# Kernel optimization log

Hardware: AMD Instinct MI355X
Metric: run time of the kernel (lower is better)

## Reference

```python
import jax, jax.numpy as jnp
import numpy as np

B, IN, K, E = 2048, 1024, 128, 64  # batch, in_features, n_concepts, emb_size


def setup_inputs() -> dict:
    key = jax.random.key(0)
    k1, k2, k3, k4, k5 = jax.random.split(key, 5)
    x = jax.random.normal(k1, (B, IN), dtype=jnp.float32)
    # stacked per-concept Linear(in_features, 2*emb_size)
    W = jax.random.normal(k2, (K, IN, 2 * E), dtype=jnp.float32) * (1.0 / np.sqrt(IN))
    b = jax.random.normal(k3, (K, 2 * E), dtype=jnp.float32) * 0.01
    # shared prob predictor Linear(2*emb_size, 1)
    wp = jax.random.normal(k4, (2 * E,), dtype=jnp.float32) * (1.0 / np.sqrt(2 * E))
    bp = jax.random.normal(k5, (), dtype=jnp.float32) * 0.01
    return {"x": x, "W": W, "b": b, "wp": wp, "bp": bp}


def reference(x, W, b, wp, bp):
    # batched GEMM over all concepts at once: [B,K,2E]
    context = jax.nn.leaky_relu(jnp.einsum('bi,kio->bko', x, W) + b)
    # shared predictor + sigmoid: [B,K]
    c_pred = jax.nn.sigmoid(jnp.einsum('bko,o->bk', context, wp) + bp)
    ctx_pos = context[..., :E]
    ctx_neg = context[..., E:]
    p = c_pred[..., None]
    c_emb = ctx_pos * p + ctx_neg * (1.0 - p)  # [B,K,E]
    return c_emb, c_pred
```

## Files before the change

kernel.cpp:

```cpp
#include <hip/hip_runtime.h>

typedef unsigned int u32;
typedef unsigned short u16;
typedef __attribute__((ext_vector_type(8))) __bf16 bf16x8;
typedef __attribute__((ext_vector_type(4))) float f32x4;

#define B_SZ 2048
#define IN_SZ 1024
#define K_SZ 128
#define E_SZ 64
#define TWOE 128
static const size_t OUT_EMB = (size_t)B_SZ * K_SZ * E_SZ;

__device__ __forceinline__ u16 f2bf(float f) {
    u32 u = __builtin_bit_cast(u32, f);
    u32 r = u + 0x7fffu + ((u >> 16) & 1u);
    return (u16)(r >> 16);
}

__device__ __forceinline__ void async16(const void* g, void* l) {
    __builtin_amdgcn_global_load_lds((const __attribute__((address_space(1))) u32*)g,
                                     (__attribute__((address_space(3))) u32*)l, 16, 0, 0);
}

__global__ void __launch_bounds__(256) cvt_x(const float* __restrict__ in, u16* __restrict__ outp, int n4) {
    int i = blockIdx.x * blockDim.x + threadIdx.x;
    if (i < n4) {
        float4 v = ((const float4*)in)[i];
        u32 lo = (u32)f2bf(v.x) | ((u32)f2bf(v.y) << 16);
        u32 hi = (u32)f2bf(v.z) | ((u32)f2bf(v.w) << 16);
        ((uint2*)outp)[i] = make_uint2(lo, hi);
    }
}

__global__ void __launch_bounds__(256) cvt_w(const float* __restrict__ W, u16* __restrict__ wt) {
    __shared__ u16 tr[128][72];
    const int k = blockIdx.y, i0 = blockIdx.x * 64;
    const float* src = W + (size_t)k * IN_SZ * TWOE + (size_t)i0 * TWOE;
#pragma unroll
    for (int r = 0; r < 8; ++r) {
        int idx = r * 256 + threadIdx.x;
        int i = idx >> 5;
        int o = (idx & 31) * 4;
        float4 v = ((const float4*)src)[idx];
        tr[o + 0][i] = f2bf(v.x);
        tr[o + 1][i] = f2bf(v.y);
        tr[o + 2][i] = f2bf(v.z);
        tr[o + 3][i] = f2bf(v.w);
    }
    __syncthreads();
    const int o = threadIdx.x >> 1, h = threadIdx.x & 1;
    u16* dst = wt + ((size_t)(k * TWOE + o) * IN_SZ) + i0 + h * 32;
#pragma unroll
    for (int s = 0; s < 4; ++s) {
        uint4 v = *(const uint4*)&tr[o][h * 32 + s * 8];
        ((uint4*)dst)[s] = v;
    }
}

__global__ void __launch_bounds__(256) cvt_pred(const float* __restrict__ pw, float* __restrict__ out) {
    __shared__ float t[128][132];
    const int b0 = blockIdx.x * 128;
    const int tid = threadIdx.x;
#pragma unroll
    for (int i = 0; i < 16; ++i) {
        int idx = i * 256 + tid;
        int kk = idx >> 5, c4 = (idx & 31) * 4;
        float4 v = *(const float4*)(pw + (size_t)kk * B_SZ + b0 + c4);
        t[kk][c4 + 0] = v.x; t[kk][c4 + 1] = v.y; t[kk][c4 + 2] = v.z; t[kk][c4 + 3] = v.w;
    }
    __syncthreads();
#pragma unroll
    for (int i = 0; i < 16; ++i) {
        int idx = i * 256 + tid;
        int bl = idx >> 5, k4 = (idx & 31) * 4;
        float4 v = make_float4(t[k4 + 0][bl], t[k4 + 1][bl], t[k4 + 2][bl], t[k4 + 3][bl]);
        *(float4*)(out + OUT_EMB + (size_t)(b0 + bl) * K_SZ + k4) = v;
    }
}

__global__ void __launch_bounds__(512, 2) fused_main(
    const u16* __restrict__ xb,
    const u16* __restrict__ wt,
    const float* __restrict__ bias, const float* __restrict__ wpv,
    const float* __restrict__ bpp, float* __restrict__ out,
    float* __restrict__ pw) {
    __shared__ u16 smst[32768];
    char* smb = (char*)&smst[0];

    const int tid = threadIdx.x;
    const int l = tid & 63, w = tid >> 6;
    const int wm = w >> 2, wn = w & 3;
    const int hi = l >> 4, lo16 = l & 15;
    const int q = l >> 2;
    const int swz = (l & 3) ^ ((l >> 3) & 3);

    const int id = blockIdx.x;
    const int xcd = id & 7, j = id >> 3;
    const int kp = (xcd << 3) | (j >> 3);
    const int brow = (j & 7) << 8;

    const u16* abase = wt + ((size_t)kp * 256 + w * 16 + q) * IN_SZ + swz * 8;
    const u16* bbase = xb + (size_t)(brow + w * 16 + q) * IN_SZ + swz * 8;

    const int xsl = (hi ^ ((lo16 >> 1) & 3)) << 4;

    f32x4 acc[8][4] = {};

    auto SA = [&](int d, int tp) {
        u16* dst = &smst[0] + d * 8192 + w * 512;
        const u16* src = abase + tp * 32;
        async16(src, dst);
        async16(src + (size_t)128 * IN_SZ, dst + 4096);
    };
    auto SB = [&](int d, int tp) {
        u16* dst = &smst[0] + 16384 + d * 8192 + w * 512;
        const u16* src = bbase + tp * 32;
        async16(src, dst);
        async16(src + (size_t)128 * IN_SZ, dst + 4096);
    };

    auto PHN = [&](int d) {
        const char* ra = smb + d * 16384;
        const char* rb = smb + 32768 + d * 16384;
        bf16x8 af[8], bfr[4];
#pragma unroll
        for (int n = 0; n < 4; ++n)
            bfr[n] = *(const bf16x8*)(rb + (wn * 64 + n * 16 + lo16) * 64 + xsl);
#pragma unroll
        for (int mm = 0; mm < 8; ++mm)
            af[mm] = *(const bf16x8*)(ra + (wm * 128 + mm * 16 + lo16) * 64 + xsl);
        __builtin_amdgcn_s_setprio(1);
#pragma unroll
        for (int mm = 0; mm < 8; ++mm)
#pragma unroll
            for (int n = 0; n < 4; ++n)
                acc[mm][n] = __builtin_amdgcn_mfma_f32_16x16x32_bf16(
                    af[mm], bfr[n], acc[mm][n], 0, 0, 0);
        __builtin_amdgcn_s_setprio(0);
    };

    SA(0, 0); SB(0, 0);
    asm volatile("s_waitcnt vmcnt(0)" ::: "memory");
    __builtin_amdgcn_s_barrier();

#pragma unroll 1
    for (int t = 0; t < 32; ++t) {
        const int d = t & 1;
        if (t < 31) {
            SA(d ^ 1, t + 1); SB(d ^ 1, t + 1);
            asm volatile("" ::: "memory");
        }
        PHN(d);
        asm volatile("s_waitcnt vmcnt(0)" ::: "memory");
        __builtin_amdgcn_s_barrier();
    }

    const int kglob = kp * 2 + wm;
    const float bp_val = *bpp;
    float4 b4[8], w4[8];
#pragma unroll
    for (int m = 0; m < 8; ++m) {
        b4[m] = *(const float4*)(bias + kglob * TWOE + m * 16 + hi * 4);
        w4[m] = *(const float4*)(wpv + m * 16 + hi * 4);
    }
    float pn[4];
#pragma unroll
    for (int n = 0; n < 4; ++n) {
        float s = 0.f;
#pragma unroll
        for (int m = 0; m < 8; ++m) {
            f32x4 v = acc[m][n];
            float t0 = v[0] + b4[m].x; t0 = t0 > 0.f ? t0 : 0.01f * t0;
            float t1 = v[1] + b4[m].y; t1 = t1 > 0.f ? t1 : 0.01f * t1;
            float t2 = v[2] + b4[m].z; t2 = t2 > 0.f ? t2 : 0.01f * t2;
            float t3 = v[3] + b4[m].w; t3 = t3 > 0.f ? t3 : 0.01f * t3;
            v[0] = t0; v[1] = t1; v[2] = t2; v[3] = t3;
            acc[m][n] = v;
            s += t0 * w4[m].x + t1 * w4[m].y + t2 * w4[m].z + t3 * w4[m].w;
        }
        s += __shfl_xor(s, 16);
        s += __shfl_xor(s, 32);
        pn[n] = 1.f / (1.f + __expf(-(s + bp_val)));
    }
    if (hi == 0) {
        if (pw) {
#pragma unroll
            for (int n = 0; n < 4; ++n)
                pw[(size_t)kglob * B_SZ + brow + wn * 64 + n * 16 + lo16] = pn[n];
        } else {
#pragma unroll
            for (int n = 0; n < 4; ++n)
                out[OUT_EMB + (size_t)(brow + wn * 64 + n * 16 + lo16) * K_SZ + kglob] = pn[n];
        }
    }
#pragma unroll
    for (int n = 0; n < 4; ++n) {
        const size_t bb = (size_t)(brow + wn * 64 + n * 16 + lo16);
        float* op = out + (bb * K_SZ + kglob) * E_SZ + hi * 4;
        const float pv = pn[n], qv = 1.f - pn[n];
#pragma unroll
        for (int mp = 0; mp < 4; ++mp) {
            f32x4 cp = acc[mp][n], cn = acc[mp + 4][n];
            f32x4 r;
            r[0] = pv * cp[0] + qv * cn[0];
            r[1] = pv * cp[1] + qv * cn[1];
            r[2] = pv * cp[2] + qv * cn[2];
            r[3] = pv * cp[3] + qv * cn[3];
            *(f32x4*)(op + mp * 16) = r;
        }
    }
}

__global__ void __launch_bounds__(128) fallback_kernel(
    const float* __restrict__ x, const float* __restrict__ W,
    const float* __restrict__ bias, const float* __restrict__ wpv,
    const float* __restrict__ bpp, float* __restrict__ out) {
    const int k = blockIdx.y;
    const int b0 = blockIdx.x * 8;
    const int o = threadIdx.x;
    __shared__ float xs[8][1024];
    __shared__ float red[2];
    __shared__ float exch[64];
    for (int idx = threadIdx.x; idx < 8 * 1024; idx += 128)
        xs[idx >> 10][idx & 1023] = x[(size_t)(b0 + (idx >> 10)) * IN_SZ + (idx & 1023)];
    __syncthreads();
    float a[8] = {};
    for (int i = 0; i < 1024; ++i) {
        float wv = W[((size_t)k * IN_SZ + i) * TWOE + o];
#pragma unroll
        for (int bb = 0; bb < 8; ++bb) a[bb] += xs[bb][i] * wv;
    }
    const float bo = bias[k * TWOE + o], wo = wpv[o], bpv = *bpp;
    for (int bb = 0; bb < 8; ++bb) {
        float c = a[bb] + bo;
        c = c > 0.f ? c : 0.01f * c;
        float s = c * wo;
        for (int off = 1; off < 64; off <<= 1) s += __shfl_xor(s, off);
        if ((threadIdx.x & 63) == 0) red[threadIdx.x >> 6] = s;
        __syncthreads();
        float p = 1.f / (1.f + expf(-(red[0] + red[1] + bpv)));
        if (o >= 64) exch[o - 64] = (1.f - p) * c;
        __syncthreads();
        if (o < 64) out[((size_t)(b0 + bb) * K_SZ + k) * E_SZ + o] = p * c + exch[o];
        if (o == 0) out[OUT_EMB + (size_t)(b0 + bb) * K_SZ + k] = p;
        __syncthreads();
    }
}

extern "C" void kernel_launch(void* const* d_in, const int* in_sizes, int n_in,
                              void* d_out, int out_size, void* d_ws, size_t ws_size,
                              hipStream_t stream) {
    const float* x = (const float*)d_in[0];
    const float* W = (const float*)d_in[1];
    const float* bias = (const float*)d_in[2];
    const float* wp = (const float*)d_in[3];
    const float* bp = (const float*)d_in[4];
    float* out = (float*)d_out;

    const size_t X_ELEMS = (size_t)B_SZ * IN_SZ;
    const size_t WT_ELEMS = (size_t)K_SZ * TWOE * IN_SZ;
    const size_t PW_ELEMS = (size_t)K_SZ * B_SZ;
    const size_t NEED_BASE = (X_ELEMS + WT_ELEMS) * sizeof(u16);
    const size_t NEED_FULL = NEED_BASE + PW_ELEMS * sizeof(float);

    if (ws_size >= NEED_BASE) {
        u16* xb = (u16*)d_ws;
        u16* wt = xb + X_ELEMS;
        float* pw = (ws_size >= NEED_FULL) ? (float*)(wt + WT_ELEMS) : nullptr;
        int n4 = (int)(X_ELEMS / 4);
        cvt_x<<<dim3((n4 + 255) / 256), 256, 0, stream>>>(x, xb, n4);
        cvt_w<<<dim3(16, 128), 256, 0, stream>>>(W, wt);
        fused_main<<<dim3(512), 512, 0, stream>>>(xb, wt, bias, wp, bp, out, pw);
        if (pw) cvt_pred<<<dim3(16), 256, 0, stream>>>(pw, out);
    } else {
        fallback_kernel<<<dim3(B_SZ / 8, K_SZ), 128, 0, stream>>>(x, W, bias, wp, bp, out);
    }
}
```

Baseline: 108.4 us.

## Merge x/W bf16 conversion kernels and deepen GEMM prefetch to two stages

Combines the separate x and W fp32→bf16 conversion kernels into one launch with extra grid rows for x, removing one kernel launch and its tail. The main GEMM loop now prefetches two K-tiles ahead. Each iteration issues the load for tile t+2 into the buffer it has just read into registers, then waits with vmcnt(4) instead of vmcnt(0), so global loads overlap more with the MFMA work. The cost is an extra barrier per iteration after the LDS reads, plus the need for correct vmcnt accounting.

```diff
diff --git a/kernel.cpp b/kernel.cpp
--- a/kernel.cpp
+++ b/kernel.cpp
@@ -23,38 +23,43 @@
                                      (__attribute__((address_space(3))) u32*)l, 16, 0, 0);
 }
 
-__global__ void __launch_bounds__(256) cvt_x(const float* __restrict__ in, u16* __restrict__ outp, int n4) {
-    int i = blockIdx.x * blockDim.x + threadIdx.x;
-    if (i < n4) {
-        float4 v = ((const float4*)in)[i];
-        u32 lo = (u32)f2bf(v.x) | ((u32)f2bf(v.y) << 16);
-        u32 hi = (u32)f2bf(v.z) | ((u32)f2bf(v.w) << 16);
-        ((uint2*)outp)[i] = make_uint2(lo, hi);
-    }
-}
-
-__global__ void __launch_bounds__(256) cvt_w(const float* __restrict__ W, u16* __restrict__ wt) {
-    __shared__ u16 tr[128][72];
-    const int k = blockIdx.y, i0 = blockIdx.x * 64;
-    const float* src = W + (size_t)k * IN_SZ * TWOE + (size_t)i0 * TWOE;
-#pragma unroll
-    for (int r = 0; r < 8; ++r) {
-        int idx = r * 256 + threadIdx.x;
-        int i = idx >> 5;
-        int o = (idx & 31) * 4;
-        float4 v = ((const float4*)src)[idx];
-        tr[o + 0][i] = f2bf(v.x);
-        tr[o + 1][i] = f2bf(v.y);
-        tr[o + 2][i] = f2bf(v.z);
-        tr[o + 3][i] = f2bf(v.w);
-    }
-    __syncthreads();
-    const int o = threadIdx.x >> 1, h = threadIdx.x & 1;
-    u16* dst = wt + ((size_t)(k * TWOE + o) * IN_SZ) + i0 + h * 32;
-#pragma unroll
-    for (int s = 0; s < 4; ++s) {
-        uint4 v = *(const uint4*)&tr[o][h * 32 + s * 8];
-        ((uint4*)dst)[s] = v;
+__global__ void __launch_bounds__(256) cvt_xw(const float* __restrict__ W, u16* __restrict__ wt,
+                                              const float* __restrict__ x, u16* __restrict__ xb) {
+    const int tid = threadIdx.x;
+    if (blockIdx.y < 128) {
+        __shared__ u16 tr[128][72];
+        const int k = blockIdx.y, i0 = blockIdx.x * 64;
+        const float* src = W + (size_t)k * IN_SZ * TWOE + (size_t)i0 * TWOE;
+#pragma unroll
+        for (int r = 0; r < 8; ++r) {
+            int idx = r * 256 + tid;
+            int i = idx >> 5;
+            int o = (idx & 31) * 4;
+            float4 v = ((const float4*)src)[idx];
+            tr[o + 0][i] = f2bf(v.x);
+            tr[o + 1][i] = f2bf(v.y);
+            tr[o + 2][i] = f2bf(v.z);
+            tr[o + 3][i] = f2bf(v.w);
+        }
+        __syncthreads();
+        const int o = tid >> 1, h = tid & 1;
+        u16* dst = wt + ((size_t)(k * TWOE + o) * IN_SZ) + i0 + h * 32;
+#pragma unroll
+        for (int s = 0; s < 4; ++s) {
+            uint4 v = *(const uint4*)&tr[o][h * 32 + s * 8];
+            ((uint4*)dst)[s] = v;
+        }
+    } else {
+        const int chunk = (blockIdx.y - 128) * 16 + blockIdx.x;
+        const int base = chunk * 4096;
+#pragma unroll
+        for (int s = 0; s < 16; ++s) {
+            int i = base + s * 256 + tid;
+            float4 v = ((const float4*)x)[i];
+            u32 lo = (u32)f2bf(v.x) | ((u32)f2bf(v.y) << 16);
+            u32 hi = (u32)f2bf(v.z) | ((u32)f2bf(v.w) << 16);
+            ((uint2*)xb)[i] = make_uint2(lo, hi);
+        }
     }
 }
 
@@ -120,7 +125,14 @@
         async16(src + (size_t)128 * IN_SZ, dst + 4096);
     };
 
-    auto PHN = [&](int d) {
+    SA(0, 0); SB(0, 0);
+    SA(1, 1); SB(1, 1);
+    asm volatile("s_waitcnt vmcnt(4)" ::: "memory");
+    __builtin_amdgcn_s_barrier();
+
+#pragma unroll 1
+    for (int t = 0; t < 32; ++t) {
+        const int d = t & 1;
         const char* ra = smb + d * 16384;
         const char* rb = smb + 32768 + d * 16384;
         bf16x8 af[8], bfr[4];
@@ -130,6 +142,13 @@
 #pragma unroll
         for (int mm = 0; mm < 8; ++mm)
             af[mm] = *(const bf16x8*)(ra + (wm * 128 + mm * 16 + lo16) * 64 + xsl);
+        asm volatile("s_waitcnt lgkmcnt(0)" ::: "memory");
+        __builtin_amdgcn_s_barrier();
+        __builtin_amdgcn_sched_barrier(0);
+        if (t < 30) {
+            SA(d, t + 2); SB(d, t + 2);
+            asm volatile("" ::: "memory");
+        }
         __builtin_amdgcn_s_setprio(1);
 #pragma unroll
         for (int mm = 0; mm < 8; ++mm)
@@ -138,21 +157,8 @@
                 acc[mm][n] = __builtin_amdgcn_mfma_f32_16x16x32_bf16(
                     af[mm], bfr[n], acc[mm][n], 0, 0, 0);
         __builtin_amdgcn_s_setprio(0);
-    };
-
-    SA(0, 0); SB(0, 0);
-    asm volatile("s_waitcnt vmcnt(0)" ::: "memory");
-    __builtin_amdgcn_s_barrier();
-
-#pragma unroll 1
-    for (int t = 0; t < 32; ++t) {
-        const int d = t & 1;
-        if (t < 31) {
-            SA(d ^ 1, t + 1); SB(d ^ 1, t + 1);
-            asm volatile("" ::: "memory");
-        }
-        PHN(d);
-        asm volatile("s_waitcnt vmcnt(0)" ::: "memory");
+        if (t < 30) asm volatile("s_waitcnt vmcnt(4)" ::: "memory");
+        else        asm volatile("s_waitcnt vmcnt(0)" ::: "memory");
         __builtin_amdgcn_s_barrier();
     }
 
@@ -268,9 +274,7 @@
         u16* xb = (u16*)d_ws;
         u16* wt = xb + X_ELEMS;
         float* pw = (ws_size >= NEED_FULL) ? (float*)(wt + WT_ELEMS) : nullptr;
-        int n4 = (int)(X_ELEMS / 4);
-        cvt_x<<<dim3((n4 + 255) / 256), 256, 0, stream>>>(x, xb, n4);
-        cvt_w<<<dim3(16, 128), 256, 0, stream>>>(W, wt);
+        cvt_xw<<<dim3(16, 136), 256, 0, stream>>>(W, wt, x, xb);
         fused_main<<<dim3(512), 512, 0, stream>>>(xb, wt, bias, wp, bp, out, pw);
         if (pw) cvt_pred<<<dim3(16), 256, 0, stream>>>(pw, out);
     } else {
```

Result: no change. 108.1 us (-0.3%).
